# Kernel optimization log

Hardware: AMD Instinct MI355X
Metric: run time of the kernel (lower is better)

## Reference

```python
import jax, jax.numpy as jnp
import numpy as np


def setup_inputs() -> dict:
    key = jax.random.key(0)
    ks = jax.random.split(key, 5)
    B, H, S, C, Dh = 2, 16, 2048, 2048, 64
    HID = H * Dh
    return {
        "q": jax.random.normal(ks[0], (B, H, S, Dh), dtype=jnp.float32),
        "k": jax.random.normal(ks[1], (B, H, C + S, Dh), dtype=jnp.float32),
        "v": jax.random.normal(ks[2], (B, H, C + S, Dh), dtype=jnp.float32),
        "memory_length": 256,
        "W": jax.random.normal(ks[3], (HID, HID), dtype=jnp.float32) / np.sqrt(HID),
        "b": jax.random.normal(ks[4], (HID,), dtype=jnp.float32) * 0.01,
    }


def _build_mask(S, KV, memory_length):
    # KV = CACHE_LEN + S; columns >= CACHE_LEN + memory_length are restricted.
    C = KV - S
    rows = jnp.arange(S)[:, None]          # query position in [0, S)
    cols = jnp.arange(KV)[None, :]         # key position in [0, KV)
    restricted = cols >= (C + memory_length)
    # memory rows (< memory_length) never see restricted cols;
    # other rows: strictly-upper-triangular masking (col - (C+mem) > row - mem)
    mem_row = rows < memory_length
    future = (cols - (C + memory_length)) > (rows - memory_length)
    return (restricted & (mem_row | future))  # bool [S, KV], True = masked


def reference(q, k, v, memory_length, W, b):
    B, H, S, Dh = q.shape
    KV = k.shape[2]
    HID = H * Dh
    scale = 1.0 / np.sqrt(Dh).astype(np.float32)
    scores = jnp.einsum('bhsd,bhtd->bhst', q, k) * scale   # [B,H,S,KV]
    mask2d = _build_mask(S, KV, memory_length)             # [S,KV] bool
    scores = jnp.where(mask2d[None, None], -jnp.inf, scores)
    attn_w = jax.nn.softmax(scores, axis=-1)
    attn = jnp.einsum('bhst,bhtd->bshd', attn_w, v).reshape(B, S, HID)
    out = attn @ W.T + b
    # torch module returns full [B,H,S,KV] float mask of 0/1
    mask_full = jnp.broadcast_to(mask2d.astype(q.dtype), (B, H, S, KV))
    return out, mask_full
```

## Files before the change

### kernel.cpp

```cpp
#include <hip/hip_runtime.h>
#include <hip/hip_bf16.h>
#include <math.h>

typedef __bf16 bf16;
typedef __bf16 bf16x4 __attribute__((ext_vector_type(4)));
typedef __bf16 bf16x8 __attribute__((ext_vector_type(8)));
typedef float f32x4 __attribute__((ext_vector_type(4)));

#define MFMA(a, b, c) __builtin_amdgcn_mfma_f32_16x16x32_bf16((a), (b), (c), 0, 0, 0)

constexpr int Bb  = 2;
constexpr int Hh  = 16;
constexpr int Ss  = 2048;
constexpr int KVv = 4096;
constexpr int Dd  = 64;
constexpr int Cc  = KVv - Ss;
constexpr int HID = Hh * Dd;

constexpr float QSCL = 0.125f * 1.44269504088896340736f;

constexpr size_t MASK_F4   = (size_t)Bb * Hh * Ss * KVv / 4;
constexpr size_t SCR_BYTES = 16777216ull + 16777216ull + 2097152ull + 8388608ull;
constexpr size_t M2_F4     = MASK_F4 - (2097152ull + 8388608ull) / 16;
constexpr size_t M1_F4     = 44000000;

__device__ __forceinline__ void write_mask_range(
    float* __restrict__ mout, int mem, size_t lo, size_t hi,
    int mblk, int nmblk, int tid, int nthr)
{
    const int R = Cc + mem;
    const size_t stride = (size_t)nmblk * nthr;
    for (size_t i = lo + (size_t)mblk * nthr + tid; i < hi; i += stride) {
        size_t flat = i * 4;
        int t = (int)(flat & (size_t)(KVv - 1));
        int s = (int)((flat >> 12) & (size_t)(Ss - 1));
        int thr = (s < mem) ? R : (s + Cc + 1);
        f32x4 vv;
        vv[0] = (float)(t >= thr);
        vv[1] = (float)(t + 1 >= thr);
        vv[2] = (float)(t + 2 >= thr);
        vv[3] = (float)(t + 3 >= thr);
        __builtin_nontemporal_store(vv, (f32x4*)(mout + flat));
    }
}

__global__ __launch_bounds__(256) void prep_kernel(
    const float* __restrict__ K, const float* __restrict__ W,
    const float* __restrict__ V,
    bf16* __restrict__ Kb, bf16* __restrict__ Wb, bf16* __restrict__ Vt)
{
    const int bid = blockIdx.x;
    if (bid < 2048) {
        __shared__ __align__(16) bf16 T[64][72];
        const int bh = bid >> 6;
        const int t0 = (bid & 63) * 64;
        const int row = threadIdx.x >> 2;
        const int cg  = threadIdx.x & 3;
        const float* vb = V + (size_t)bh * KVv * Dd + (size_t)(t0 + row) * Dd + cg * 16;
        float4 x0 = ((const float4*)vb)[0];
        float4 x1 = ((const float4*)vb)[1];
        float4 x2 = ((const float4*)vb)[2];
        float4 x3 = ((const float4*)vb)[3];
        float xs[16] = {x0.x,x0.y,x0.z,x0.w, x1.x,x1.y,x1.z,x1.w,
                        x2.x,x2.y,x2.z,x2.w, x3.x,x3.y,x3.z,x3.w};
#pragma unroll
        for (int j = 0; j < 16; ++j)
            T[cg * 16 + j][row] = (bf16)xs[j];
        __syncthreads();
        const int d = row;
        bf16* o = Vt + (size_t)bh * Dd * KVv + (size_t)d * KVv + t0 + cg * 16;
        ((bf16x8*)o)[0] = *(const bf16x8*)&T[d][cg * 16];
        ((bf16x8*)o)[1] = *(const bf16x8*)&T[d][cg * 16 + 8];
        return;
    }
    const size_t nK4 = (size_t)Bb * Hh * KVv * Dd / 4;
    const size_t nW4 = (size_t)HID * HID / 4;
    const size_t total = nK4 + nW4;
    const size_t stride = (size_t)(gridDim.x - 2048) * 256;
    for (size_t i = (size_t)(bid - 2048) * 256 + threadIdx.x; i < total; i += stride) {
        float4 x = (i < nK4) ? ((const float4*)K)[i] : ((const float4*)W)[i - nK4];
        bf16x4 t;
        t[0] = (bf16)x.x; t[1] = (bf16)x.y; t[2] = (bf16)x.z; t[3] = (bf16)x.w;
        if (i < nK4) ((bf16x4*)Kb)[i] = t;
        else         ((bf16x4*)Wb)[i - nK4] = t;
    }
}

template <bool MASKED>
__device__ __forceinline__ void kv_tile(
    int t0, const bf16* __restrict__ kb_p, const bf16* __restrict__ vt_p,
    const bf16x8 qa[2], const int thr[4], int tid, int lr, int lg,
    bf16 (*__restrict__ Klds)[72], bf16 (*__restrict__ Vlds)[72],
    bf16 (*__restrict__ Pw)[72], f32x4 acco[4], float lsum[4])
{
    {
        const int row = tid >> 3, c8 = tid & 7;
        bf16x8 kx = *(const bf16x8*)(kb_p + (size_t)(t0 + row) * Dd + c8 * 8);
        bf16x8 vx = *(const bf16x8*)(vt_p + (size_t)row * KVv + t0 + c8 * 8);
        *(bf16x8*)&Klds[row][c8 * 8] = kx;
        *(bf16x8*)&Vlds[row][c8 * 8] = vx;
    }
    __syncthreads();

    f32x4 accs[4];
#pragma unroll
    for (int kg = 0; kg < 4; ++kg) accs[kg] = (f32x4){0.f, 0.f, 0.f, 0.f};
    __builtin_amdgcn_s_setprio(1);
#pragma unroll
    for (int ks = 0; ks < 2; ++ks) {
#pragma unroll
        for (int kg = 0; kg < 4; ++kg) {
            bf16x8 kf = *(const bf16x8*)&Klds[kg * 16 + lr][ks * 32 + lg * 8];
            accs[kg] = MFMA(qa[ks], kf, accs[kg]);
        }
    }
    __builtin_amdgcn_s_setprio(0);

#pragma unroll
    for (int r = 0; r < 4; ++r) {
#pragma unroll
        for (int kg = 0; kg < 4; ++kg) {
            float sl = accs[kg][r];
            if (MASKED) {
                int tcol = t0 + kg * 16 + lr;
                sl = (tcol < thr[r]) ? sl : -1e30f;
            }
            accs[kg][r] = __builtin_amdgcn_exp2f(sl);
        }
        lsum[r] += (accs[0][r] + accs[1][r]) + (accs[2][r] + accs[3][r]);
#pragma unroll
        for (int kg = 0; kg < 4; ++kg)
            Pw[lg * 4 + r][kg * 16 + lr] = (bf16)accs[kg][r];
    }
    asm volatile("s_waitcnt lgkmcnt(0)" ::: "memory");

    __builtin_amdgcn_s_setprio(1);
#pragma unroll
    for (int ks = 0; ks < 2; ++ks) {
        bf16x8 pa = *(const bf16x8*)&Pw[lr][ks * 32 + lg * 8];
#pragma unroll
        for (int dg = 0; dg < 4; ++dg) {
            bf16x8 vf = *(const bf16x8*)&Vlds[dg * 16 + lr][ks * 32 + lg * 8];
            acco[dg] = MFMA(pa, vf, acco[dg]);
        }
    }
    __builtin_amdgcn_s_setprio(0);
    __syncthreads();
}

__global__ __launch_bounds__(512) void fused_attn_kernel(
    const float* __restrict__ q, const bf16* __restrict__ Kb,
    const bf16* __restrict__ Vtb, const int* __restrict__ memp,
    bf16* __restrict__ attnb, float* __restrict__ mout)
{
    __shared__ __align__(16) bf16 Klds[64][72];
    __shared__ __align__(16) bf16 Vlds[64][72];
    __shared__ __align__(16) bf16 Plds[8][16][72];

    const int fid = blockIdx.x;
    const int mem = *memp;
    if (fid >= 512) {
        write_mask_range(mout, mem, 0, M1_F4, fid - 512, gridDim.x - 512,
                         threadIdx.x, 512);
        return;
    }
    const int xcd = fid & 7;
    const int slot = fid >> 3;
    const int qblk = slot & 15;
    const int bh = (slot >> 4) * 8 + xcd;

    const int tid = threadIdx.x;
    const int w  = tid >> 6;
    const int l  = tid & 63;
    const int lr = l & 15;
    const int lg = l >> 4;
    const int q0 = qblk * 128;
    const int R = Cc + mem;

    const float* qp   = q   + (size_t)bh * Ss * Dd;
    const bf16*  kb_p = Kb  + (size_t)bh * KVv * Dd;
    const bf16*  vt_p = Vtb + (size_t)bh * Dd * KVv;

    const int qrow = q0 + w * 16 + lr;
    bf16x8 qa[2];
#pragma unroll
    for (int ks = 0; ks < 2; ++ks) {
        const float* p8 = qp + (size_t)qrow * Dd + ks * 32 + lg * 8;
        float4 x0 = *(const float4*)p8;
        float4 x1 = *(const float4*)(p8 + 4);
        bf16x8 a;
        a[0] = (bf16)(x0.x * QSCL); a[1] = (bf16)(x0.y * QSCL);
        a[2] = (bf16)(x0.z * QSCL); a[3] = (bf16)(x0.w * QSCL);
        a[4] = (bf16)(x1.x * QSCL); a[5] = (bf16)(x1.y * QSCL);
        a[6] = (bf16)(x1.z * QSCL); a[7] = (bf16)(x1.w * QSCL);
        qa[ks] = a;
    }

    int thr[4];
#pragma unroll
    for (int r = 0; r < 4; ++r) {
        int qabs = q0 + w * 16 + lg * 4 + r;
        thr[r] = (qabs < mem) ? R : (qabs + Cc + 1);
    }
    const int qmaxb = q0 + 127;
    int kv_end = (qmaxb < mem) ? R : (qmaxb + Cc + 1);
    if (kv_end > KVv) kv_end = KVv;
    int thr_min = (q0 < mem) ? R : (q0 + Cc + 1);
    int p1_end = thr_min & ~63;
    if (p1_end > kv_end) p1_end = kv_end;

    f32x4 acco[4];
#pragma unroll
    for (int dg = 0; dg < 4; ++dg) acco[dg] = (f32x4){0.f, 0.f, 0.f, 0.f};
    float lsum[4] = {0.f, 0.f, 0.f, 0.f};

    for (int t0 = 0; t0 < p1_end; t0 += 64)
        kv_tile<false>(t0, kb_p, vt_p, qa, thr, tid, lr, lg, Klds, Vlds, Plds[w], acco, lsum);
    for (int t0 = p1_end; t0 < kv_end; t0 += 64)
        kv_tile<true>(t0, kb_p, vt_p, qa, thr, tid, lr, lg, Klds, Vlds, Plds[w], acco, lsum);

    const int b = bh >> 4, h = bh & 15;
#pragma unroll
    for (int r = 0; r < 4; ++r) {
        float s = lsum[r];
        s += __shfl_xor(s, 1);
        s += __shfl_xor(s, 2);
        s += __shfl_xor(s, 4);
        s += __shfl_xor(s, 8);
        float inv = 1.f / s;
        int qabs = q0 + w * 16 + lg * 4 + r;
        bf16* dst = attnb + (size_t)(b * Ss + qabs) * HID + h * Dd;
#pragma unroll
        for (int dg = 0; dg < 4; ++dg)
            dst[dg * 16 + lr] = (bf16)(acco[dg][r] * inv);
    }
}

__global__ __launch_bounds__(256) void fused_proj_kernel(
    const bf16* __restrict__ A, const bf16* __restrict__ Wb,
    const float* __restrict__ bias, float* __restrict__ out,
    const int* __restrict__ memp, float* __restrict__ mout, size_t mhi)
{
    __shared__ __align__(16) bf16 Alds[64][72];
    __shared__ __align__(16) bf16 Wlds[64][72];

    const int fid = blockIdx.x;
    if (fid >= 1024) {
        write_mask_range(mout, *memp, M1_F4, mhi, fid - 1024, gridDim.x - 1024,
                         threadIdx.x, 256);
        return;
    }
    const int xcd = fid & 7;
    const int slot = fid >> 3;
    const int o0 = ((slot & 1) * 8 + xcd) * 64;
    const int i0 = (slot >> 1) * 64;

    const int tid = threadIdx.x;
    const int w  = tid >> 6;
    const int l  = tid & 63;
    const int lr = l & 15;
    const int lg = l >> 4;

    f32x4 acc[4];
#pragma unroll
    for (int og = 0; og < 4; ++og) acc[og] = (f32x4){0.f, 0.f, 0.f, 0.f};

    for (int kc = 0; kc < HID; kc += 64) {
        const int row = tid >> 2, cg = tid & 3;
        bf16x8 a0 = ((const bf16x8*)(A  + (size_t)(i0 + row) * HID + kc + cg * 16))[0];
        bf16x8 a1 = ((const bf16x8*)(A  + (size_t)(i0 + row) * HID + kc + cg * 16))[1];
        bf16x8 w0 = ((const bf16x8*)(Wb + (size_t)(o0 + row) * HID + kc + cg * 16))[0];
        bf16x8 w1 = ((const bf16x8*)(Wb + (size_t)(o0 + row) * HID + kc + cg * 16))[1];
        *(bf16x8*)&Alds[row][cg * 16]     = a0;
        *(bf16x8*)&Alds[row][cg * 16 + 8] = a1;
        *(bf16x8*)&Wlds[row][cg * 16]     = w0;
        *(bf16x8*)&Wlds[row][cg * 16 + 8] = w1;
        __syncthreads();
        __builtin_amdgcn_s_setprio(1);
#pragma unroll
        for (int ks = 0; ks < 2; ++ks) {
            bf16x8 af = *(const bf16x8*)&Alds[w * 16 + lr][ks * 32 + lg * 8];
#pragma unroll
            for (int og = 0; og < 4; ++og) {
                bf16x8 wf = *(const bf16x8*)&Wlds[og * 16 + lr][ks * 32 + lg * 8];
                acc[og] = MFMA(af, wf, acc[og]);
            }
        }
        __builtin_amdgcn_s_setprio(0);
        __syncthreads();
    }

#pragma unroll
    for (int r = 0; r < 4; ++r) {
        int i = i0 + w * 16 + lg * 4 + r;
#pragma unroll
        for (int og = 0; og < 4; ++og) {
            int o = o0 + og * 16 + lr;
            __builtin_nontemporal_store(acc[og][r] + bias[o], &out[(size_t)i * HID + o]);
        }
    }
}

__global__ __launch_bounds__(256) void mask_tail_kernel(
    float* __restrict__ mout, const int* __restrict__ memp)
{
    write_mask_range(mout, *memp, M2_F4, MASK_F4, blockIdx.x, gridDim.x,
                     threadIdx.x, 256);
}

extern "C" void kernel_launch(void* const* d_in, const int* in_sizes, int n_in,
                              void* d_out, int out_size, void* d_ws, size_t ws_size,
                              hipStream_t stream)
{
    (void)in_sizes; (void)n_in; (void)out_size;
    const float* q    = (const float*)d_in[0];
    const float* k    = (const float*)d_in[1];
    const float* v    = (const float*)d_in[2];
    const int*   memp = (const int*)d_in[3];
    const float* W    = (const float*)d_in[4];
    const float* bias = (const float*)d_in[5];

    float* out     = (float*)d_out;
    float* maskout = out + (size_t)Bb * Ss * HID;

    const bool use_ws = ws_size >= SCR_BYTES;
    char* scr = use_ws ? (char*)d_ws
                       : (char*)maskout + MASK_F4 * 16 - SCR_BYTES;
    bf16* Kbf   = (bf16*)scr;
    bf16* Vtb   = Kbf + (size_t)Bb * Hh * KVv * Dd;
    bf16* Wbf   = Vtb + (size_t)Bb * Hh * KVv * Dd;
    bf16* attnb = Wbf + (size_t)HID * HID;

    const size_t mhi = use_ws ? MASK_F4 : M2_F4;

    prep_kernel<<<dim3(2048 + 1024), 256, 0, stream>>>(k, W, v, Kbf, Wbf, Vtb);
    fused_attn_kernel<<<dim3(512 + 1024), 512, 0, stream>>>(q, Kbf, Vtb, memp, attnb, maskout);
    fused_proj_kernel<<<dim3(1024 + 512), 256, 0, stream>>>(attnb, Wbf, bias, out, memp, maskout, mhi);
    if (!use_ws)
        mask_tail_kernel<<<dim3(256), 256, 0, stream>>>(maskout, memp);
}
```

Before: 268.4 us.

## Double-buffer KV tiles, convert W inline in projection, widen mask stores

The attention loop becomes a single loop with double-buffered K/V LDS tiles. The next tile is prefetched into registers while the current one is computed, which removes one barrier per tile. The separate masked and unmasked tile paths are merged, so every tile now pays the mask compare. W is no longer converted to bf16 in the prep kernel; the projection kernel loads fp32 W and converts it inline, trading a prep pass for more bytes and conversion work per tile. Mask writes now emit two float4 stores per thread iteration, and the prep and tail grids are resized to fit the smaller scratch area.

```diff
diff --git a/kernel.cpp b/kernel.cpp
--- a/kernel.cpp
+++ b/kernel.cpp
@@ -20,34 +20,35 @@
 constexpr float QSCL = 0.125f * 1.44269504088896340736f;
 
 constexpr size_t MASK_F4   = (size_t)Bb * Hh * Ss * KVv / 4;
-constexpr size_t SCR_BYTES = 16777216ull + 16777216ull + 2097152ull + 8388608ull;
-constexpr size_t M2_F4     = MASK_F4 - (2097152ull + 8388608ull) / 16;
+constexpr size_t SCR_BYTES = 16777216ull + 16777216ull + 8388608ull;
+constexpr size_t M2_F4     = MASK_F4 - SCR_BYTES / 16;
 constexpr size_t M1_F4     = 44000000;
 
 __device__ __forceinline__ void write_mask_range(
-    float* __restrict__ mout, int mem, size_t lo, size_t hi,
+    float* __restrict__ mout, int mem, size_t lo4, size_t hi4,
     int mblk, int nmblk, int tid, int nthr)
 {
     const int R = Cc + mem;
+    const size_t lo = lo4 >> 1, hi = hi4 >> 1;
     const size_t stride = (size_t)nmblk * nthr;
-    for (size_t i = lo + (size_t)mblk * nthr + tid; i < hi; i += stride) {
-        size_t flat = i * 4;
+    for (size_t p = lo + (size_t)mblk * nthr + tid; p < hi; p += stride) {
+        size_t flat = p * 8;
         int t = (int)(flat & (size_t)(KVv - 1));
         int s = (int)((flat >> 12) & (size_t)(Ss - 1));
         int thr = (s < mem) ? R : (s + Cc + 1);
-        f32x4 vv;
-        vv[0] = (float)(t >= thr);
-        vv[1] = (float)(t + 1 >= thr);
-        vv[2] = (float)(t + 2 >= thr);
-        vv[3] = (float)(t + 3 >= thr);
-        __builtin_nontemporal_store(vv, (f32x4*)(mout + flat));
+        f32x4 v0, v1;
+        v0[0] = (float)(t     >= thr); v0[1] = (float)(t + 1 >= thr);
+        v0[2] = (float)(t + 2 >= thr); v0[3] = (float)(t + 3 >= thr);
+        v1[0] = (float)(t + 4 >= thr); v1[1] = (float)(t + 5 >= thr);
+        v1[2] = (float)(t + 6 >= thr); v1[3] = (float)(t + 7 >= thr);
+        __builtin_nontemporal_store(v0, (f32x4*)(mout + flat));
+        __builtin_nontemporal_store(v1, (f32x4*)(mout + flat + 4));
     }
 }
 
 __global__ __launch_bounds__(256) void prep_kernel(
-    const float* __restrict__ K, const float* __restrict__ W,
-    const float* __restrict__ V,
-    bf16* __restrict__ Kb, bf16* __restrict__ Wb, bf16* __restrict__ Vt)
+    const float* __restrict__ K, const float* __restrict__ V,
+    bf16* __restrict__ Kb, bf16* __restrict__ Vt)
 {
     const int bid = blockIdx.x;
     if (bid < 2048) {
@@ -74,78 +75,13 @@
         return;
     }
     const size_t nK4 = (size_t)Bb * Hh * KVv * Dd / 4;
-    const size_t nW4 = (size_t)HID * HID / 4;
-    const size_t total = nK4 + nW4;
     const size_t stride = (size_t)(gridDim.x - 2048) * 256;
-    for (size_t i = (size_t)(bid - 2048) * 256 + threadIdx.x; i < total; i += stride) {
-        float4 x = (i < nK4) ? ((const float4*)K)[i] : ((const float4*)W)[i - nK4];
+    for (size_t i = (size_t)(bid - 2048) * 256 + threadIdx.x; i < nK4; i += stride) {
+        float4 x = ((const float4*)K)[i];
         bf16x4 t;
         t[0] = (bf16)x.x; t[1] = (bf16)x.y; t[2] = (bf16)x.z; t[3] = (bf16)x.w;
-        if (i < nK4) ((bf16x4*)Kb)[i] = t;
-        else         ((bf16x4*)Wb)[i - nK4] = t;
-    }
-}
-
-template <bool MASKED>
-__device__ __forceinline__ void kv_tile(
-    int t0, const bf16* __restrict__ kb_p, const bf16* __restrict__ vt_p,
-    const bf16x8 qa[2], const int thr[4], int tid, int lr, int lg,
-    bf16 (*__restrict__ Klds)[72], bf16 (*__restrict__ Vlds)[72],
-    bf16 (*__restrict__ Pw)[72], f32x4 acco[4], float lsum[4])
-{
-    {
-        const int row = tid >> 3, c8 = tid & 7;
-        bf16x8 kx = *(const bf16x8*)(kb_p + (size_t)(t0 + row) * Dd + c8 * 8);
-        bf16x8 vx = *(const bf16x8*)(vt_p + (size_t)row * KVv + t0 + c8 * 8);
-        *(bf16x8*)&Klds[row][c8 * 8] = kx;
-        *(bf16x8*)&Vlds[row][c8 * 8] = vx;
-    }
-    __syncthreads();
-
-    f32x4 accs[4];
-#pragma unroll
-    for (int kg = 0; kg < 4; ++kg) accs[kg] = (f32x4){0.f, 0.f, 0.f, 0.f};
-    __builtin_amdgcn_s_setprio(1);
-#pragma unroll
-    for (int ks = 0; ks < 2; ++ks) {
-#pragma unroll
-        for (int kg = 0; kg < 4; ++kg) {
-            bf16x8 kf = *(const bf16x8*)&Klds[kg * 16 + lr][ks * 32 + lg * 8];
-            accs[kg] = MFMA(qa[ks], kf, accs[kg]);
-        }
-    }
-    __builtin_amdgcn_s_setprio(0);
-
-#pragma unroll
-    for (int r = 0; r < 4; ++r) {
-#pragma unroll
-        for (int kg = 0; kg < 4; ++kg) {
-            float sl = accs[kg][r];
-            if (MASKED) {
-                int tcol = t0 + kg * 16 + lr;
-                sl = (tcol < thr[r]) ? sl : -1e30f;
-            }
-            accs[kg][r] = __builtin_amdgcn_exp2f(sl);
-        }
-        lsum[r] += (accs[0][r] + accs[1][r]) + (accs[2][r] + accs[3][r]);
-#pragma unroll
-        for (int kg = 0; kg < 4; ++kg)
-            Pw[lg * 4 + r][kg * 16 + lr] = (bf16)accs[kg][r];
-    }
-    asm volatile("s_waitcnt lgkmcnt(0)" ::: "memory");
-
-    __builtin_amdgcn_s_setprio(1);
-#pragma unroll
-    for (int ks = 0; ks < 2; ++ks) {
-        bf16x8 pa = *(const bf16x8*)&Pw[lr][ks * 32 + lg * 8];
-#pragma unroll
-        for (int dg = 0; dg < 4; ++dg) {
-            bf16x8 vf = *(const bf16x8*)&Vlds[dg * 16 + lr][ks * 32 + lg * 8];
-            acco[dg] = MFMA(pa, vf, acco[dg]);
-        }
-    }
-    __builtin_amdgcn_s_setprio(0);
-    __syncthreads();
+        ((bf16x4*)Kb)[i] = t;
+    }
 }
 
 __global__ __launch_bounds__(512) void fused_attn_kernel(
@@ -153,8 +89,8 @@
     const bf16* __restrict__ Vtb, const int* __restrict__ memp,
     bf16* __restrict__ attnb, float* __restrict__ mout)
 {
-    __shared__ __align__(16) bf16 Klds[64][72];
-    __shared__ __align__(16) bf16 Vlds[64][72];
+    __shared__ __align__(16) bf16 Klds[2][64][72];
+    __shared__ __align__(16) bf16 Vlds[2][64][72];
     __shared__ __align__(16) bf16 Plds[8][16][72];
 
     const int fid = blockIdx.x;
@@ -205,19 +141,79 @@
     const int qmaxb = q0 + 127;
     int kv_end = (qmaxb < mem) ? R : (qmaxb + Cc + 1);
     if (kv_end > KVv) kv_end = KVv;
-    int thr_min = (q0 < mem) ? R : (q0 + Cc + 1);
-    int p1_end = thr_min & ~63;
-    if (p1_end > kv_end) p1_end = kv_end;
+    const int nt = kv_end >> 6;
 
     f32x4 acco[4];
 #pragma unroll
     for (int dg = 0; dg < 4; ++dg) acco[dg] = (f32x4){0.f, 0.f, 0.f, 0.f};
     float lsum[4] = {0.f, 0.f, 0.f, 0.f};
 
-    for (int t0 = 0; t0 < p1_end; t0 += 64)
-        kv_tile<false>(t0, kb_p, vt_p, qa, thr, tid, lr, lg, Klds, Vlds, Plds[w], acco, lsum);
-    for (int t0 = p1_end; t0 < kv_end; t0 += 64)
-        kv_tile<true>(t0, kb_p, vt_p, qa, thr, tid, lr, lg, Klds, Vlds, Plds[w], acco, lsum);
+    const int srow = tid >> 3, sc8 = (tid & 7) * 8;
+
+    bf16x8 kreg = *(const bf16x8*)(kb_p + (size_t)srow * Dd + sc8);
+    bf16x8 vreg = *(const bf16x8*)(vt_p + (size_t)srow * KVv + sc8);
+    *(bf16x8*)&Klds[0][srow][sc8] = kreg;
+    *(bf16x8*)&Vlds[0][srow][sc8] = vreg;
+    __syncthreads();
+
+    bf16 (*__restrict__ Pw)[72] = Plds[w];
+
+    for (int it = 0; it < nt; ++it) {
+        const int t0 = it << 6;
+        const int p = it & 1;
+        const bool more = (it + 1 < nt);
+        if (more) {
+            kreg = *(const bf16x8*)(kb_p + (size_t)(t0 + 64 + srow) * Dd + sc8);
+            vreg = *(const bf16x8*)(vt_p + (size_t)srow * KVv + t0 + 64 + sc8);
+        }
+
+        f32x4 accs[4];
+#pragma unroll
+        for (int kg = 0; kg < 4; ++kg) accs[kg] = (f32x4){0.f, 0.f, 0.f, 0.f};
+        __builtin_amdgcn_s_setprio(1);
+#pragma unroll
+        for (int ks = 0; ks < 2; ++ks) {
+#pragma unroll
+            for (int kg = 0; kg < 4; ++kg) {
+                bf16x8 kf = *(const bf16x8*)&Klds[p][kg * 16 + lr][ks * 32 + lg * 8];
+                accs[kg] = MFMA(qa[ks], kf, accs[kg]);
+            }
+        }
+        __builtin_amdgcn_s_setprio(0);
+
+#pragma unroll
+        for (int r = 0; r < 4; ++r) {
+#pragma unroll
+            for (int kg = 0; kg < 4; ++kg) {
+                int tcol = t0 + kg * 16 + lr;
+                float sl = (tcol < thr[r]) ? accs[kg][r] : -1e30f;
+                accs[kg][r] = __builtin_amdgcn_exp2f(sl);
+            }
+            lsum[r] += (accs[0][r] + accs[1][r]) + (accs[2][r] + accs[3][r]);
+#pragma unroll
+            for (int kg = 0; kg < 4; ++kg)
+                Pw[lg * 4 + r][kg * 16 + lr] = (bf16)accs[kg][r];
+        }
+        asm volatile("s_waitcnt lgkmcnt(0)" ::: "memory");
+
+        __builtin_amdgcn_s_setprio(1);
+#pragma unroll
+        for (int ks = 0; ks < 2; ++ks) {
+            bf16x8 pa = *(const bf16x8*)&Pw[lr][ks * 32 + lg * 8];
+#pragma unroll
+            for (int dg = 0; dg < 4; ++dg) {
+                bf16x8 vf = *(const bf16x8*)&Vlds[p][dg * 16 + lr][ks * 32 + lg * 8];
+                acco[dg] = MFMA(pa, vf, acco[dg]);
+            }
+        }
+        __builtin_amdgcn_s_setprio(0);
+
+        if (more) {
+            *(bf16x8*)&Klds[p ^ 1][srow][sc8] = kreg;
+            *(bf16x8*)&Vlds[p ^ 1][srow][sc8] = vreg;
+        }
+        __syncthreads();
+    }
 
     const int b = bh >> 4, h = bh & 15;
 #pragma unroll
@@ -237,7 +233,7 @@
 }
 
 __global__ __launch_bounds__(256) void fused_proj_kernel(
-    const bf16* __restrict__ A, const bf16* __restrict__ Wb,
+    const bf16* __restrict__ A, const float* __restrict__ W,
     const float* __restrict__ bias, float* __restrict__ out,
     const int* __restrict__ memp, float* __restrict__ mout, size_t mhi)
 {
@@ -266,15 +262,24 @@
     for (int og = 0; og < 4; ++og) acc[og] = (f32x4){0.f, 0.f, 0.f, 0.f};
 
     for (int kc = 0; kc < HID; kc += 64) {
-        const int row = tid >> 2, cg = tid & 3;
-        bf16x8 a0 = ((const bf16x8*)(A  + (size_t)(i0 + row) * HID + kc + cg * 16))[0];
-        bf16x8 a1 = ((const bf16x8*)(A  + (size_t)(i0 + row) * HID + kc + cg * 16))[1];
-        bf16x8 w0 = ((const bf16x8*)(Wb + (size_t)(o0 + row) * HID + kc + cg * 16))[0];
-        bf16x8 w1 = ((const bf16x8*)(Wb + (size_t)(o0 + row) * HID + kc + cg * 16))[1];
-        *(bf16x8*)&Alds[row][cg * 16]     = a0;
-        *(bf16x8*)&Alds[row][cg * 16 + 8] = a1;
-        *(bf16x8*)&Wlds[row][cg * 16]     = w0;
-        *(bf16x8*)&Wlds[row][cg * 16 + 8] = w1;
+        const int row = tid >> 2, c16 = (tid & 3) * 16;
+        const bf16* ap = A + (size_t)(i0 + row) * HID + kc + c16;
+        bf16x8 a0 = ((const bf16x8*)ap)[0];
+        bf16x8 a1 = ((const bf16x8*)ap)[1];
+        const float* wp = W + (size_t)(o0 + row) * HID + kc + c16;
+        float4 w0 = ((const float4*)wp)[0];
+        float4 w1 = ((const float4*)wp)[1];
+        float4 w2 = ((const float4*)wp)[2];
+        float4 w3 = ((const float4*)wp)[3];
+        bf16x8 wlo, whi;
+        wlo[0] = (bf16)w0.x; wlo[1] = (bf16)w0.y; wlo[2] = (bf16)w0.z; wlo[3] = (bf16)w0.w;
+        wlo[4] = (bf16)w1.x; wlo[5] = (bf16)w1.y; wlo[6] = (bf16)w1.z; wlo[7] = (bf16)w1.w;
+        whi[0] = (bf16)w2.x; whi[1] = (bf16)w2.y; whi[2] = (bf16)w2.z; whi[3] = (bf16)w2.w;
+        whi[4] = (bf16)w3.x; whi[5] = (bf16)w3.y; whi[6] = (bf16)w3.z; whi[7] = (bf16)w3.w;
+        *(bf16x8*)&Alds[row][c16]     = a0;
+        *(bf16x8*)&Alds[row][c16 + 8] = a1;
+        *(bf16x8*)&Wlds[row][c16]     = wlo;
+        *(bf16x8*)&Wlds[row][c16 + 8] = whi;
         __syncthreads();
         __builtin_amdgcn_s_setprio(1);
 #pragma unroll
@@ -325,17 +330,16 @@
 
     const bool use_ws = ws_size >= SCR_BYTES;
     char* scr = use_ws ? (char*)d_ws
-                       : (char*)maskout + MASK_F4 * 16 - SCR_BYTES;
+                       : (char*)maskout + M2_F4 * 16;
     bf16* Kbf   = (bf16*)scr;
     bf16* Vtb   = Kbf + (size_t)Bb * Hh * KVv * Dd;
-    bf16* Wbf   = Vtb + (size_t)Bb * Hh * KVv * Dd;
-    bf16* attnb = Wbf + (size_t)HID * HID;
+    bf16* attnb = Vtb + (size_t)Bb * Hh * KVv * Dd;
 
     const size_t mhi = use_ws ? MASK_F4 : M2_F4;
 
-    prep_kernel<<<dim3(2048 + 1024), 256, 0, stream>>>(k, W, v, Kbf, Wbf, Vtb);
+    prep_kernel<<<dim3(2048 + 512), 256, 0, stream>>>(k, v, Kbf, Vtb);
     fused_attn_kernel<<<dim3(512 + 1024), 512, 0, stream>>>(q, Kbf, Vtb, memp, attnb, maskout);
-    fused_proj_kernel<<<dim3(1024 + 512), 256, 0, stream>>>(attnb, Wbf, bias, out, memp, maskout, mhi);
+    fused_proj_kernel<<<dim3(1024 + 512), 256, 0, stream>>>(attnb, W, bias, out, memp, maskout, mhi);
     if (!use_ws)
-        mask_tail_kernel<<<dim3(256), 256, 0, stream>>>(maskout, memp);
-}
+        mask_tail_kernel<<<dim3(192), 256, 0, stream>>>(maskout, memp);
+}
```

New measurement: 620.7 us. 2.31x slower.
